# Optimization experiments

Measured on AMD Instinct MI355X. Metric: run time of the kernel, lower is better.

## Reference

```python
import jax, jax.numpy as jnp
import numpy as np

IDIM = 128   # idim == odim (fc1 input dim must match shift-slice width idim_q)
HDIM = 1024
CDIM = 256
IGNORE_OUT = 10000.0


def setup_inputs() -> dict:
    key = jax.random.key(0)
    ks = jax.random.split(key, 4)
    B, T = 4, 512
    x = jax.random.normal(ks[0], (B, T, IDIM), dtype=jnp.float32)
    y = jax.random.normal(ks[1], (B, T, IDIM), dtype=jnp.float32)
    # xavier-ish init for the two linears (bias zeroed, as in initialize())
    w1 = jax.random.normal(ks[2], (HDIM, IDIM), dtype=jnp.float32) / np.sqrt(IDIM).astype(np.float32)
    b1 = jnp.zeros((HDIM,), jnp.float32)
    w2 = jax.random.normal(ks[3], (IDIM, HDIM), dtype=jnp.float32) / np.sqrt(HDIM).astype(np.float32)
    b2 = jnpts = jnp.zeros((IDIM,), jnp.float32)
    return {"x": x, "y": y, "w1": w1, "b1": b1, "w2": w2, "b2": b2}


def _shift_stack(key_seq, idim):
    """Vectorized _pad_for_shift: (B,T,idim) -> (B,T,2*idim-1,idim) shifted slices."""
    pad = idim - 1
    kp = jnp.pad(key_seq, ((0, 0), (0, 0), (pad, pad)))  # (B,T,3*idim-2)
    idx = jnp.arange(2 * idim - 1)[:, None] + jnp.arange(idim)[None, :]  # (S, idim)
    return kp[..., idx]  # (B,T,S,idim)


def _forward(x, y, w1, b1, w2, b2):
    idim = IDIM
    n_iter = HDIM // CDIM
    seq_mask = (y == IGNORE_OUT)                      # (B,T,odim)
    denom = jnp.sum(~seq_mask).astype(x.dtype)
    y_res, x_res = y, x
    losses = []
    for i in range(n_iter):
        # --- argaug (scale=False): sliding cosine cross-correlation + argmax ---
        kpt = _shift_stack(x_res, idim)               # (B,T,S,idim), S=2*idim-1
        num = jnp.einsum('btd,btsd->bts', y_res, kpt)
        den = jnp.linalg.norm(y_res, axis=-1)[..., None] * jnp.linalg.norm(kpt, axis=-1)
        sim = jnp.where(den == 0, 0.0, num / jnp.where(den == 0, 1.0, den))  # NaN(0/0) -> 0
        idx = jnp.argmax(sim, axis=-1)                # (B,T), first max like torch.max
        x_aug = jnp.take_along_axis(kpt, idx[..., None, None], axis=2)[..., 0, :]  # (B,T,idim)
        # --- attention (detached) ---
        attn = jax.lax.stop_gradient(jax.nn.softmax(x_aug * y_res, axis=-1))
        x_attn = x_aug * attn
        # --- _reverse_pad_for_shift: un-shift x_attn by 2*idim-2 - idx ---
        pad = idim - 1
        xap = jnp.pad(x_attn, ((0, 0), (0, 0), (pad, pad)))
        ridx = (2 * idim - 2 - idx)[..., None] + jnp.arange(idim)  # (B,T,idim)
        x_ele = jnp.take_along_axis(xap, ridx, axis=-1)
        # --- channel-masked two-layer MLP ---
        h = x_attn @ w1.T + b1                        # (B,T,hdim)
        m = jnp.zeros((HDIM,), x.dtype).at[i * CDIM:(i + 1) * CDIM].set(1.0)
        y_ele = (h * m) @ w2.T + b2                   # (B,T,odim)
        # --- masked MSE (sum of masked squared errors / #unmasked) ---
        sq = jnp.where(seq_mask, 0.0, (y_ele - y_res) ** 2)
        losses.append(jnp.sum(sq) / denom)
        y_res = y_res - y_ele
        x_res = x_res - x_ele
    return jnp.mean(jnp.stack(losses))


def reference(x, y, w1, b1, w2, b2):
    return _forward(x, y, w1, b1, w2, b2)
```

## Files before the change

kernel.cpp:

```cpp
#include <hip/hip_runtime.h>
#include <math.h>

#define NROWS 2048
#define NBLK  2048
#define NITER 4
#define IGNORE_OUT 10000.0f
#define LOG2E 1.44269504088896340736f

__device__ __forceinline__ float readlanef(float v, int lane){
  return __int_as_float(__builtin_amdgcn_readlane(__float_as_int(v), lane));
}

__device__ __forceinline__ float waveScanInc(float v){
  v += __int_as_float(__builtin_amdgcn_update_dpp(0, __float_as_int(v), 0x111, 0xF, 0xF, true));
  v += __int_as_float(__builtin_amdgcn_update_dpp(0, __float_as_int(v), 0x112, 0xF, 0xF, true));
  v += __int_as_float(__builtin_amdgcn_update_dpp(0, __float_as_int(v), 0x114, 0xF, 0xF, true));
  v += __int_as_float(__builtin_amdgcn_update_dpp(0, __float_as_int(v), 0x118, 0xF, 0xF, true));
  v += __int_as_float(__builtin_amdgcn_update_dpp(0, __float_as_int(v), 0x142, 0xA, 0xF, true));
  v += __int_as_float(__builtin_amdgcn_update_dpp(0, __float_as_int(v), 0x143, 0xC, 0xF, true));
  return v;
}
__device__ __forceinline__ float waveSum(float v){
  return readlanef(waveScanInc(v), 63);
}
__device__ __forceinline__ void waveArgmax(float &v, int &i){
#define AMSTEP(ctrl, rm) { \
    float ov = __int_as_float(__builtin_amdgcn_update_dpp(__float_as_int(v), __float_as_int(v), ctrl, rm, 0xF, false)); \
    int   oi = __builtin_amdgcn_update_dpp(i, i, ctrl, rm, 0xF, false); \
    bool take = (ov > v) || (ov == v && oi < i); \
    v = take ? ov : v; i = take ? oi : i; }
  AMSTEP(0x111, 0xF) AMSTEP(0x112, 0xF) AMSTEP(0x114, 0xF)
  AMSTEP(0x118, 0xF) AMSTEP(0x142, 0xA) AMSTEP(0x143, 0xC)
#undef AMSTEP
  v = readlanef(v, 63);
  i = __builtin_amdgcn_readlane(i, 63);
}
__device__ __forceinline__ void gatherPair(float v0, float v1, int idx, float &a, float &b){
  int c = idx & 63;
  float g0 = __shfl(v0, c, 64);
  float g1 = __shfl(v1, c, 64);
  a = ((unsigned)idx < 128u) ? ((idx & 64) ? g1 : g0) : 0.f;
  int idx2 = idx + 64;
  b = ((unsigned)idx2 < 128u) ? ((idx2 & 64) ? g1 : g0) : 0.f;
}

__global__ __launch_bounds__(128)
void prepK(const float* __restrict__ w1, const float* __restrict__ b1,
           const float* __restrict__ w2, const float* __restrict__ b2,
           float* __restrict__ M4, float* __restrict__ biasT, int* __restrict__ ticket){
  const int blk = blockIdx.x;
  const int u = threadIdx.x;
  if (blk < 512){
    int i = blk >> 7, o = blk & 127;
    const float* w1p = w1 + (i * 256) * 128 + u;
    const float* w2p = w2 + o * 1024 + i * 256;
    float a = 0.f;
    #pragma unroll 16
    for (int c = 0; c < 256; ++c) a = fmaf(w1p[c * 128], w2p[c], a);
    M4[i * 16384 + (u >> 2) * 512 + o * 4 + (u & 3)] = a;
  } else if (blk < 516){
    int i = blk - 512;
    const float* w2p = w2 + u * 1024 + i * 256;
    const float* b1p = b1 + i * 256;
    float a = b2[u];
    #pragma unroll 8
    for (int c = 0; c < 256; ++c) a = fmaf(b1p[c], w2p[c], a);
    biasT[i * 128 + u] = a;
  } else {
    if (u == 0) *ticket = 0;
  }
}

__global__ __launch_bounds__(128, 4)
void mainK(const float* __restrict__ x, const float* __restrict__ y,
           const float* __restrict__ M4, const float* __restrict__ biasT,
           unsigned long long* __restrict__ partials, int* __restrict__ ticket,
           float* __restrict__ out){
  __shared__ float yd[384];
  __shared__ float sVal[2];
  __shared__ int   sIdx[2];
  __shared__ float sL[2], sC[2];
  __shared__ int   sOld;

  const int u = threadIdx.x;
  const int l = u & 63;
  const int w = u >> 6;
  const long base = (long)blockIdx.x * 128;

  float xlo = x[base + l], xhi = x[base + 64 + l];
  float ylo = y[base + l], yhi = y[base + 64 + l];
  const float yOwn0 = w ? yhi : ylo;
  const bool mOwn = (yOwn0 == IGNORE_OUT);
  float cnt = mOwn ? 0.f : 1.f;
  float lossAcc = 0.f;

  yd[128 + u] = yOwn0; yd[256 + u] = yOwn0;
  __syncthreads();

  for (int i = 0; i < NITER; ++i){
    float own2 = w ? xhi * xhi : xlo * xlo;
    float oth2 = w ? xlo * xlo : xhi * xhi;
    float v = waveScanInc(own2);
    float osum  = waveSum(oth2);
    float total = readlanef(v, 63) + osum;
    float pref_t = w ? (v + osum) : v;

    float ny2 = waveSum(ylo * ylo + yhi * yhi);

    const float* wp = yd + (255 - u);
    float nt, n1 = 0.f;
    if (w == 0){
      float c = 0.f;
      #pragma unroll 8
      for (int j = 0; j < 64; ++j){
        c = fmaf(wp[j], readlanef(xlo, j), c);
        n1 = (j == l) ? c : n1;
      }
      float s0 = 0.f, s1 = 0.f, s2 = 0.f, s3 = 0.f;
      #pragma unroll 8
      for (int j = 0; j < 64; j += 4){
        s0 = fmaf(wp[64 + j + 0], readlanef(xhi, j + 0), s0);
        s1 = fmaf(wp[64 + j + 1], readlanef(xhi, j + 1), s1);
        s2 = fmaf(wp[64 + j + 2], readlanef(xhi, j + 2), s2);
        s3 = fmaf(wp[64 + j + 3], readlanef(xhi, j + 3), s3);
      }
      nt = c + ((s0 + s1) + (s2 + s3));
    } else {
      float s0 = 0.f, s1 = 0.f, s2 = 0.f, s3 = 0.f;
      #pragma unroll 8
      for (int j = 0; j < 64; j += 4){
        s0 = fmaf(wp[j + 0], readlanef(xlo, j + 0), s0);
        s1 = fmaf(wp[j + 1], readlanef(xlo, j + 1), s1);
        s2 = fmaf(wp[j + 2], readlanef(xlo, j + 2), s2);
        s3 = fmaf(wp[j + 3], readlanef(xlo, j + 3), s3);
      }
      float c = (s0 + s1) + (s2 + s3);
      n1 = c;
      #pragma unroll 8
      for (int j = 0; j < 64; ++j){
        c = fmaf(wp[64 + j], readlanef(xhi, j), c);
        n1 = (j == l) ? c : n1;
      }
      nt = c;
    }

    {
      bool yz = (ny2 == 0.f);
      float rNY = __builtin_amdgcn_rsqf(ny2);
      float nx2b = fmaxf(total - pref_t, 0.f);
      float s1v = (yz || pref_t == 0.f) ? 0.f : n1 * __builtin_amdgcn_rsqf(pref_t) * rNY;
      float s2v = (yz || nx2b  == 0.f) ? 0.f : (nt - n1) * __builtin_amdgcn_rsqf(nx2b) * rNY;
      if (u == 127) s2v = -INFINITY;
      float bv = s1v; int bi = u;
      if (s2v > bv){ bv = s2v; bi = u + 128; }
      waveArgmax(bv, bi);
      if (l == 0){ sVal[w] = bv; sIdx[w] = bi; }
    }
    __syncthreads();
    int sstar;
    {
      float v0 = sVal[0], v1 = sVal[1];
      int   i0 = sIdx[0], i1 = sIdx[1];
      sstar = (v1 > v0 || (v1 == v0 && i1 < i0)) ? i1 : i0;
    }

    float xa, xb;
    gatherPair(xlo, xhi, sstar + l - 127, xa, xb);
    float ea = __builtin_amdgcn_exp2f(xa * ylo * LOG2E);
    float eb = __builtin_amdgcn_exp2f(xb * yhi * LOG2E);
    float rse = __builtin_amdgcn_rcpf(waveSum(ea + eb));
    float wlo = xa * (ea * rse), whi = xb * (eb * rse);

    {
      float ga, gb;
      gatherPair(wlo, whi, l + 127 - sstar, ga, gb);
      xlo -= ga; xhi -= gb;
    }

    float ye;
    {
      const float4* Mp = (const float4*)(M4 + (size_t)i * 16384);
      float a0 = 0.f, a1 = 0.f, a2 = 0.f, a3 = 0.f;
      #pragma unroll 4
      for (int dd = 0; dd < 16; dd += 4){
        float4 m0 = Mp[(dd + 0) * 128 + u];
        float4 m1 = Mp[(dd + 1) * 128 + u];
        float4 m2 = Mp[(dd + 2) * 128 + u];
        float4 m3 = Mp[(dd + 3) * 128 + u];
        a0 = fmaf(m0.x, readlanef(wlo, 4*dd + 0), a0); a0 = fmaf(m0.y, readlanef(wlo, 4*dd + 1), a0);
        a0 = fmaf(m0.z, readlanef(wlo, 4*dd + 2), a0); a0 = fmaf(m0.w, readlanef(wlo, 4*dd + 3), a0);
        a1 = fmaf(m1.x, readlanef(wlo, 4*dd + 4), a1); a1 = fmaf(m1.y, readlanef(wlo, 4*dd + 5), a1);
        a1 = fmaf(m1.z, readlanef(wlo, 4*dd + 6), a1); a1 = fmaf(m1.w, readlanef(wlo, 4*dd + 7), a1);
        a2 = fmaf(m2.x, readlanef(wlo, 4*dd + 8), a2); a2 = fmaf(m2.y, readlanef(wlo, 4*dd + 9), a2);
        a2 = fmaf(m2.z, readlanef(wlo, 4*dd +10), a2); a2 = fmaf(m2.w, readlanef(wlo, 4*dd +11), a2);
        a3 = fmaf(m3.x, readlanef(wlo, 4*dd +12), a3); a3 = fmaf(m3.y, readlanef(wlo, 4*dd +13), a3);
        a3 = fmaf(m3.z, readlanef(wlo, 4*dd +14), a3); a3 = fmaf(m3.w, readlanef(wlo, 4*dd +15), a3);
      }
      #pragma unroll 4
      for (int dd = 16; dd < 32; dd += 4){
        float4 m0 = Mp[(dd + 0) * 128 + u];
        float4 m1 = Mp[(dd + 1) * 128 + u];
        float4 m2 = Mp[(dd + 2) * 128 + u];
        float4 m3 = Mp[(dd + 3) * 128 + u];
        int b = 4*dd - 64;
        a0 = fmaf(m0.x, readlanef(whi, b + 0), a0); a0 = fmaf(m0.y, readlanef(whi, b + 1), a0);
        a0 = fmaf(m0.z, readlanef(whi, b + 2), a0); a0 = fmaf(m0.w, readlanef(whi, b + 3), a0);
        a1 = fmaf(m1.x, readlanef(whi, b + 4), a1); a1 = fmaf(m1.y, readlanef(whi, b + 5), a1);
        a1 = fmaf(m1.z, readlanef(whi, b + 6), a1); a1 = fmaf(m1.w, readlanef(whi, b + 7), a1);
        a2 = fmaf(m2.x, readlanef(whi, b + 8), a2); a2 = fmaf(m2.y, readlanef(whi, b + 9), a2);
        a2 = fmaf(m2.z, readlanef(whi, b +10), a2); a2 = fmaf(m2.w, readlanef(whi, b +11), a2);
        a3 = fmaf(m3.x, readlanef(whi, b +12), a3); a3 = fmaf(m3.y, readlanef(whi, b +13), a3);
        a3 = fmaf(m3.z, readlanef(whi, b +14), a3); a3 = fmaf(m3.w, readlanef(whi, b +15), a3);
      }
      ye = ((a0 + a1) + (a2 + a3)) + biasT[i * 128 + u];
    }

    {
      float yOwn = w ? yhi : ylo;
      float df = ye - yOwn;
      if (!mOwn) lossAcc = fmaf(df, df, lossAcc);
      float yNew = yOwn - ye;
      yd[128 + u] = yNew; yd[256 + u] = yNew;
    }
    __syncthreads();
    ylo = yd[128 + l];
    yhi = yd[192 + l];
  }

  lossAcc = waveSum(lossAcc);
  cnt     = waveSum(cnt);
  if (l == 0){ sL[w] = lossAcc; sC[w] = cnt; }
  __syncthreads();
  if (u == 0){
    union { float2 f; unsigned long long v; } pk;
    pk.f.x = sL[0] + sL[1];
    pk.f.y = sC[0] + sC[1];
    __hip_atomic_store(&partials[blockIdx.x], pk.v, __ATOMIC_RELEASE, __HIP_MEMORY_SCOPE_AGENT);
    sOld = __hip_atomic_fetch_add(ticket, 1, __ATOMIC_ACQ_REL, __HIP_MEMORY_SCOPE_AGENT);
  }
  __syncthreads();
  if (sOld == NBLK - 1){
    float ls = 0.f, cs = 0.f;
    for (int g = u; g < NBLK; g += 128){
      union { float2 f; unsigned long long v; } pk;
      pk.v = __hip_atomic_load(&partials[g], __ATOMIC_ACQUIRE, __HIP_MEMORY_SCOPE_AGENT);
      ls += pk.f.x; cs += pk.f.y;
    }
    ls = waveSum(ls); cs = waveSum(cs);
    if (l == 0){ sL[w] = ls; sC[w] = cs; }
    __syncthreads();
    if (u == 0) out[0] = (sL[0] + sL[1]) / ((float)NITER * (sC[0] + sC[1]));
  }
}

extern "C" void kernel_launch(void* const* d_in, const int* in_sizes, int n_in,
                              void* d_out, int out_size, void* d_ws, size_t ws_size,
                              hipStream_t stream){
  const float* x  = (const float*)d_in[0];
  const float* y  = (const float*)d_in[1];
  const float* w1 = (const float*)d_in[2];
  const float* b1 = (const float*)d_in[3];
  const float* w2 = (const float*)d_in[4];
  const float* b2 = (const float*)d_in[5];
  float* out = (float*)d_out;

  int*   ticket = (int*)d_ws;
  float* M4     = (float*)((char*)d_ws + 256);
  float* biasT  = (float*)((char*)d_ws + 256 + 4 * 128 * 128 * sizeof(float));
  unsigned long long* partials =
      (unsigned long long*)((char*)d_ws + 256 + 4 * 128 * 128 * sizeof(float) + 4 * 128 * sizeof(float));

  prepK<<<517, 128, 0, stream>>>(w1, b1, w2, b2, M4, biasT, ticket);
  mainK<<<NBLK, 128, 0, stream>>>(x, y, M4, biasT, partials, ticket, out);
}
```

Baseline: 152.5 us.

## Replace readlane broadcasts with LDS float4 reads and prefetch M4 tiles

```diff
diff --git a/kernel.cpp b/kernel.cpp
--- a/kernel.cpp
+++ b/kernel.cpp
@@ -54,18 +54,28 @@
     int i = blk >> 7, o = blk & 127;
     const float* w1p = w1 + (i * 256) * 128 + u;
     const float* w2p = w2 + o * 1024 + i * 256;
-    float a = 0.f;
+    float a0 = 0.f, a1 = 0.f, a2 = 0.f, a3 = 0.f;
     #pragma unroll 16
-    for (int c = 0; c < 256; ++c) a = fmaf(w1p[c * 128], w2p[c], a);
-    M4[i * 16384 + (u >> 2) * 512 + o * 4 + (u & 3)] = a;
+    for (int c = 0; c < 256; c += 4){
+      a0 = fmaf(w1p[(c + 0) * 128], w2p[c + 0], a0);
+      a1 = fmaf(w1p[(c + 1) * 128], w2p[c + 1], a1);
+      a2 = fmaf(w1p[(c + 2) * 128], w2p[c + 2], a2);
+      a3 = fmaf(w1p[(c + 3) * 128], w2p[c + 3], a3);
+    }
+    M4[i * 16384 + (u >> 2) * 512 + o * 4 + (u & 3)] = (a0 + a1) + (a2 + a3);
   } else if (blk < 516){
     int i = blk - 512;
     const float* w2p = w2 + u * 1024 + i * 256;
     const float* b1p = b1 + i * 256;
-    float a = b2[u];
+    float a0 = b2[u], a1 = 0.f, a2 = 0.f, a3 = 0.f;
     #pragma unroll 8
-    for (int c = 0; c < 256; ++c) a = fmaf(b1p[c], w2p[c], a);
-    biasT[i * 128 + u] = a;
+    for (int c = 0; c < 256; c += 4){
+      a0 = fmaf(b1p[c + 0], w2p[c + 0], a0);
+      a1 = fmaf(b1p[c + 1], w2p[c + 1], a1);
+      a2 = fmaf(b1p[c + 2], w2p[c + 2], a2);
+      a3 = fmaf(b1p[c + 3], w2p[c + 3], a3);
+    }
+    biasT[i * 128 + u] = (a0 + a1) + (a2 + a3);
   } else {
     if (u == 0) *ticket = 0;
   }
@@ -76,7 +86,9 @@
            const float* __restrict__ M4, const float* __restrict__ biasT,
            unsigned long long* __restrict__ partials, int* __restrict__ ticket,
            float* __restrict__ out){
-  __shared__ float yd[384];
+  __shared__ float ydc[4][392];
+  __shared__ float xbuf[2][128];
+  __shared__ float wbuf[2][128];
   __shared__ float sVal[2];
   __shared__ int   sIdx[2];
   __shared__ float sL[2], sC[2];
@@ -94,55 +106,76 @@
   float cnt = mOwn ? 0.f : 1.f;
   float lossAcc = 0.f;
 
-  yd[128 + u] = yOwn0; yd[256 + u] = yOwn0;
+  #pragma unroll
+  for (int r = 0; r < 4; ++r){ ydc[r][128 + u - r] = yOwn0; ydc[r][256 + u - r] = yOwn0; }
+  xbuf[w][l] = xlo; xbuf[w][64 + l] = xhi;
   __syncthreads();
 
+  const int A = 255 - u;
+  const float4* wrow = (const float4*)&ydc[A & 3][A & ~3];
+  const float4* xrow = (const float4*)&xbuf[w][0];
+  const float4* wbv  = (const float4*)&wbuf[w][0];
+
   for (int i = 0; i < NITER; ++i){
+    const float4* Mp = (const float4*)(M4 + (size_t)i * 16384);
+    float4 mb[4][4];
+    #pragma unroll
+    for (int q = 0; q < 4; ++q) mb[0][q] = Mp[q * 128 + u];
+    #pragma unroll
+    for (int q = 0; q < 4; ++q) mb[1][q] = Mp[(4 + q) * 128 + u];
+    float bias_i = biasT[i * 128 + u];
+
     float own2 = w ? xhi * xhi : xlo * xlo;
     float oth2 = w ? xlo * xlo : xhi * xhi;
     float v = waveScanInc(own2);
     float osum  = waveSum(oth2);
     float total = readlanef(v, 63) + osum;
     float pref_t = w ? (v + osum) : v;
-
     float ny2 = waveSum(ylo * ylo + yhi * yhi);
 
-    const float* wp = yd + (255 - u);
-    float nt, n1 = 0.f;
+    float s0=0.f,s1=0.f,s2=0.f,s3=0.f, t0=0.f,t1=0.f,t2=0.f,t3=0.f, p0=0.f,p1=0.f,p2=0.f,p3=0.f;
     if (w == 0){
-      float c = 0.f;
-      #pragma unroll 8
-      for (int j = 0; j < 64; ++j){
-        c = fmaf(wp[j], readlanef(xlo, j), c);
-        n1 = (j == l) ? c : n1;
-      }
-      float s0 = 0.f, s1 = 0.f, s2 = 0.f, s3 = 0.f;
-      #pragma unroll 8
-      for (int j = 0; j < 64; j += 4){
-        s0 = fmaf(wp[64 + j + 0], readlanef(xhi, j + 0), s0);
-        s1 = fmaf(wp[64 + j + 1], readlanef(xhi, j + 1), s1);
-        s2 = fmaf(wp[64 + j + 2], readlanef(xhi, j + 2), s2);
-        s3 = fmaf(wp[64 + j + 3], readlanef(xhi, j + 3), s3);
-      }
-      nt = c + ((s0 + s1) + (s2 + s3));
+      #pragma unroll
+      for (int m = 0; m < 16; ++m){
+        float4 wv = wrow[m], xv = xrow[m];
+        s0 = fmaf(wv.x, xv.x, s0); s1 = fmaf(wv.y, xv.y, s1);
+        s2 = fmaf(wv.z, xv.z, s2); s3 = fmaf(wv.w, xv.w, s3);
+        const int jb = 4 * m;
+        p0 = fmaf(wv.x, (l >= jb    ) ? xv.x : 0.f, p0);
+        p1 = fmaf(wv.y, (l >= jb + 1) ? xv.y : 0.f, p1);
+        p2 = fmaf(wv.z, (l >= jb + 2) ? xv.z : 0.f, p2);
+        p3 = fmaf(wv.w, (l >= jb + 3) ? xv.w : 0.f, p3);
+      }
+      #pragma unroll
+      for (int m = 16; m < 32; ++m){
+        float4 wv = wrow[m], xv = xrow[m];
+        t0 = fmaf(wv.x, xv.x, t0); t1 = fmaf(wv.y, xv.y, t1);
+        t2 = fmaf(wv.z, xv.z, t2); t3 = fmaf(wv.w, xv.w, t3);
+      }
     } else {
-      float s0 = 0.f, s1 = 0.f, s2 = 0.f, s3 = 0.f;
-      #pragma unroll 8
-      for (int j = 0; j < 64; j += 4){
-        s0 = fmaf(wp[j + 0], readlanef(xlo, j + 0), s0);
-        s1 = fmaf(wp[j + 1], readlanef(xlo, j + 1), s1);
-        s2 = fmaf(wp[j + 2], readlanef(xlo, j + 2), s2);
-        s3 = fmaf(wp[j + 3], readlanef(xlo, j + 3), s3);
-      }
-      float c = (s0 + s1) + (s2 + s3);
-      n1 = c;
-      #pragma unroll 8
-      for (int j = 0; j < 64; ++j){
-        c = fmaf(wp[64 + j], readlanef(xhi, j), c);
-        n1 = (j == l) ? c : n1;
-      }
-      nt = c;
-    }
+      #pragma unroll
+      for (int m = 0; m < 16; ++m){
+        float4 wv = wrow[m], xv = xrow[m];
+        s0 = fmaf(wv.x, xv.x, s0); s1 = fmaf(wv.y, xv.y, s1);
+        s2 = fmaf(wv.z, xv.z, s2); s3 = fmaf(wv.w, xv.w, s3);
+      }
+      #pragma unroll
+      for (int m = 16; m < 32; ++m){
+        float4 wv = wrow[m], xv = xrow[m];
+        t0 = fmaf(wv.x, xv.x, t0); t1 = fmaf(wv.y, xv.y, t1);
+        t2 = fmaf(wv.z, xv.z, t2); t3 = fmaf(wv.w, xv.w, t3);
+        const int jb = 4 * m - 64;
+        p0 = fmaf(wv.x, (l >= jb    ) ? xv.x : 0.f, p0);
+        p1 = fmaf(wv.y, (l >= jb + 1) ? xv.y : 0.f, p1);
+        p2 = fmaf(wv.z, (l >= jb + 2) ? xv.z : 0.f, p2);
+        p3 = fmaf(wv.w, (l >= jb + 3) ? xv.w : 0.f, p3);
+      }
+    }
+    float Sh0 = (s0 + s1) + (s2 + s3);
+    float Sh1 = (t0 + t1) + (t2 + t3);
+    float P   = (p0 + p1) + (p2 + p3);
+    float nt = Sh0 + Sh1;
+    float n1 = w ? (Sh0 + P) : P;
 
     {
       bool yz = (ny2 == 0.f);
@@ -157,6 +190,12 @@
       if (l == 0){ sVal[w] = bv; sIdx[w] = bi; }
     }
     __syncthreads();
+
+    #pragma unroll
+    for (int q = 0; q < 4; ++q) mb[2][q] = Mp[(8 + q) * 128 + u];
+    #pragma unroll
+    for (int q = 0; q < 4; ++q) mb[3][q] = Mp[(12 + q) * 128 + u];
+
     int sstar;
     {
       float v0 = sVal[0], v1 = sVal[1];
@@ -176,43 +215,26 @@
       gatherPair(wlo, whi, l + 127 - sstar, ga, gb);
       xlo -= ga; xhi -= gb;
     }
+    xbuf[w][l] = xlo; xbuf[w][64 + l] = xhi;
+    wbuf[w][l] = wlo; wbuf[w][64 + l] = whi;
 
     float ye;
     {
-      const float4* Mp = (const float4*)(M4 + (size_t)i * 16384);
       float a0 = 0.f, a1 = 0.f, a2 = 0.f, a3 = 0.f;
-      #pragma unroll 4
-      for (int dd = 0; dd < 16; dd += 4){
-        float4 m0 = Mp[(dd + 0) * 128 + u];
-        float4 m1 = Mp[(dd + 1) * 128 + u];
-        float4 m2 = Mp[(dd + 2) * 128 + u];
-        float4 m3 = Mp[(dd + 3) * 128 + u];
-        a0 = fmaf(m0.x, readlanef(wlo, 4*dd + 0), a0); a0 = fmaf(m0.y, readlanef(wlo, 4*dd + 1), a0);
-        a0 = fmaf(m0.z, readlanef(wlo, 4*dd + 2), a0); a0 = fmaf(m0.w, readlanef(wlo, 4*dd + 3), a0);
-        a1 = fmaf(m1.x, readlanef(wlo, 4*dd + 4), a1); a1 = fmaf(m1.y, readlanef(wlo, 4*dd + 5), a1);
-        a1 = fmaf(m1.z, readlanef(wlo, 4*dd + 6), a1); a1 = fmaf(m1.w, readlanef(wlo, 4*dd + 7), a1);
-        a2 = fmaf(m2.x, readlanef(wlo, 4*dd + 8), a2); a2 = fmaf(m2.y, readlanef(wlo, 4*dd + 9), a2);
-        a2 = fmaf(m2.z, readlanef(wlo, 4*dd +10), a2); a2 = fmaf(m2.w, readlanef(wlo, 4*dd +11), a2);
-        a3 = fmaf(m3.x, readlanef(wlo, 4*dd +12), a3); a3 = fmaf(m3.y, readlanef(wlo, 4*dd +13), a3);
-        a3 = fmaf(m3.z, readlanef(wlo, 4*dd +14), a3); a3 = fmaf(m3.w, readlanef(wlo, 4*dd +15), a3);
-      }
-      #pragma unroll 4
-      for (int dd = 16; dd < 32; dd += 4){
-        float4 m0 = Mp[(dd + 0) * 128 + u];
-        float4 m1 = Mp[(dd + 1) * 128 + u];
-        float4 m2 = Mp[(dd + 2) * 128 + u];
-        float4 m3 = Mp[(dd + 3) * 128 + u];
-        int b = 4*dd - 64;
-        a0 = fmaf(m0.x, readlanef(whi, b + 0), a0); a0 = fmaf(m0.y, readlanef(whi, b + 1), a0);
-        a0 = fmaf(m0.z, readlanef(whi, b + 2), a0); a0 = fmaf(m0.w, readlanef(whi, b + 3), a0);
-        a1 = fmaf(m1.x, readlanef(whi, b + 4), a1); a1 = fmaf(m1.y, readlanef(whi, b + 5), a1);
-        a1 = fmaf(m1.z, readlanef(whi, b + 6), a1); a1 = fmaf(m1.w, readlanef(whi, b + 7), a1);
-        a2 = fmaf(m2.x, readlanef(whi, b + 8), a2); a2 = fmaf(m2.y, readlanef(whi, b + 9), a2);
-        a2 = fmaf(m2.z, readlanef(whi, b +10), a2); a2 = fmaf(m2.w, readlanef(whi, b +11), a2);
-        a3 = fmaf(m3.x, readlanef(whi, b +12), a3); a3 = fmaf(m3.y, readlanef(whi, b +13), a3);
-        a3 = fmaf(m3.z, readlanef(whi, b +14), a3); a3 = fmaf(m3.w, readlanef(whi, b +15), a3);
-      }
-      ye = ((a0 + a1) + (a2 + a3)) + biasT[i * 128 + u];
+      #pragma unroll
+      for (int g = 0; g < 8; ++g){
+        float4 m0 = mb[g & 3][0], m1 = mb[g & 3][1], m2 = mb[g & 3][2], m3 = mb[g & 3][3];
+        if (g < 4){
+          #pragma unroll
+          for (int q = 0; q < 4; ++q) mb[g & 3][q] = Mp[((g + 4) * 4 + q) * 128 + u];
+        }
+        float4 b0 = wbv[4 * g + 0], b1 = wbv[4 * g + 1], b2 = wbv[4 * g + 2], b3 = wbv[4 * g + 3];
+        a0 = fmaf(m0.x, b0.x, a0); a0 = fmaf(m0.y, b0.y, a0); a0 = fmaf(m0.z, b0.z, a0); a0 = fmaf(m0.w, b0.w, a0);
+        a1 = fmaf(m1.x, b1.x, a1); a1 = fmaf(m1.y, b1.y, a1); a1 = fmaf(m1.z, b1.z, a1); a1 = fmaf(m1.w, b1.w, a1);
+        a2 = fmaf(m2.x, b2.x, a2); a2 = fmaf(m2.y, b2.y, a2); a2 = fmaf(m2.z, b2.z, a2); a2 = fmaf(m2.w, b2.w, a2);
+        a3 = fmaf(m3.x, b3.x, a3); a3 = fmaf(m3.y, b3.y, a3); a3 = fmaf(m3.z, b3.z, a3); a3 = fmaf(m3.w, b3.w, a3);
+      }
+      ye = ((a0 + a1) + (a2 + a3)) + bias_i;
     }
 
     {
@@ -220,11 +242,12 @@
       float df = ye - yOwn;
       if (!mOwn) lossAcc = fmaf(df, df, lossAcc);
       float yNew = yOwn - ye;
-      yd[128 + u] = yNew; yd[256 + u] = yNew;
+      #pragma unroll
+      for (int r = 0; r < 4; ++r){ ydc[r][128 + u - r] = yNew; ydc[r][256 + u - r] = yNew; }
     }
     __syncthreads();
-    ylo = yd[128 + l];
-    yhi = yd[192 + l];
+    ylo = ydc[0][128 + l];
+    yhi = ydc[0][192 + l];
   }
 
   lossAcc = waveSum(lossAcc);
```

New measurement: 228.7 us. 1.5x slower.
